# Performance work log

Hardware: AMD Instinct MI355X
Metric: run time of the kernel (lower is better)

## Reference

```python
import jax, jax.numpy as jnp
import numpy as np

N_QUBITS = 12
RANK = 1024
K = 4            # outcomes per qubit
D = 2 ** N_QUBITS
N_IDX = 1_000_000


def setup_inputs() -> dict:
    key = jax.random.key(0)
    k1, k2, k3, k4 = jax.random.split(key, 4)
    params = jax.random.normal(k1, (2, D, RANK), dtype=jnp.float32)
    M_real = jax.random.normal(k2, (K, 2, 2), dtype=jnp.float32)
    M_imag = jax.random.normal(k3, (K, 2, 2), dtype=jnp.float32)
    P_idxs = jax.random.randint(k4, (N_IDX,), 0, K ** N_QUBITS, dtype=jnp.int64)
    return {"params": params, "M_real": M_real, "M_imag": M_imag, "P_idxs": P_idxs}


def _qmt(rho, M, n_qubits):
    """Born rule: P[s1..sN] = Tr[(M_{s1} x ... x M_{sN}) rho].
    Sequential per-qubit contraction; T has shape [K^n, 2^(N-n), 2^(N-n)]."""
    T = rho[None, :, :]  # axes: (done outcomes, row legs j, col legs i)
    for _ in range(n_qubits):
        k, r, c = T.shape[0], T.shape[1] // 2, T.shape[2] // 2
        Tt = T.reshape(k, 2, r, 2, c)  # (k, j_n, j_rest, i_n, i_rest)
        # Tr contribution: sum_{i,j} M[s,i,j] * rho[j,i]
        T = jnp.einsum('sij,kjait->ksat', M, Tt).reshape(k * M.shape[0], r, c)
    return T.reshape(-1)  # [K^N] complex


def reference(params, M_real, M_imag, P_idxs):
    # rho = U U^H / Tr(U U^H)
    U = jax.lax.complex(params[0], params[1])            # [D, RANK] complex64
    rho = U @ U.conj().T                                  # [D, D]
    rho = rho / jnp.trace(rho)
    M = jax.lax.complex(M_real, M_imag)                   # [K, 2, 2] complex64
    P_all = _qmt(rho, M, N_QUBITS).real                   # [K^N] float32
    return P_all[P_idxs]
```

## Files before the change

### kernel.cpp

```cpp
#include <hip/hip_runtime.h>

#define D 4096
#define RANK 1024
#define K2 2048
#define UELEMS 4194304ULL
#define NTOT 16777216ULL
#define QSCALE 16000.0f

typedef __attribute__((ext_vector_type(4))) int i32x4;

__device__ float g_inv_tr[1];
__device__ float g_scale[D];

static __device__ __forceinline__ void load_lds16(const void* g, void* l) {
    __builtin_amdgcn_global_load_lds(
        (const __attribute__((address_space(1))) unsigned int*)g,
        (__attribute__((address_space(3))) unsigned int*)l, 16, 0, 0);
}

__global__ __launch_bounds__(256) void convert_w_i8(const float* __restrict__ P,
                                                    char* __restrict__ Wh,
                                                    char* __restrict__ Wl,
                                                    char* __restrict__ N2h,
                                                    char* __restrict__ N2l)
{
    const int w = threadIdx.x >> 6, lane = threadIdx.x & 63;
    const int row = blockIdx.x * 4 + w;

    float ur[16], ui[16];
    const float* pr = P + (size_t)row * RANK + lane * 16;
    const float* pi = P + UELEMS + (size_t)row * RANK + lane * 16;
    #pragma unroll
    for (int q = 0; q < 4; ++q) {
        const float4 a = ((const float4*)pr)[q];
        const float4 b = ((const float4*)pi)[q];
        ur[q * 4 + 0] = a.x; ur[q * 4 + 1] = a.y; ur[q * 4 + 2] = a.z; ur[q * 4 + 3] = a.w;
        ui[q * 4 + 0] = b.x; ui[q * 4 + 1] = b.y; ui[q * 4 + 2] = b.z; ui[q * 4 + 3] = b.w;
    }
    float mx = 0.f;
    #pragma unroll
    for (int e = 0; e < 16; ++e)
        mx = fmaxf(mx, fmaxf(fabsf(ur[e]), fabsf(ui[e])));
    #pragma unroll
    for (int off = 1; off < 64; off <<= 1)
        mx = fmaxf(mx, __shfl_xor(mx, off));
    const float inv = mx > 0.f ? QSCALE / mx : 0.f;
    if (lane == 0) g_scale[row] = mx / QSCALE;

    int hr[16], lr[16], hi[16], li[16];
    #pragma unroll
    for (int e = 0; e < 16; ++e) {
        float q = ur[e] * inv;
        float hf = rintf(q * 0.0078125f);
        hr[e] = (int)hf; lr[e] = (int)rintf(q - 128.f * hf);
        q = ui[e] * inv;
        hf = rintf(q * 0.0078125f);
        hi[e] = (int)hf; li[e] = (int)rintf(q - 128.f * hf);
    }
    uint4 phr, plr, phi, pli, pnh, pnl;
    unsigned* dst[6] = {(unsigned*)&phr, (unsigned*)&plr, (unsigned*)&phi,
                        (unsigned*)&pli, (unsigned*)&pnh, (unsigned*)&pnl};
    #pragma unroll
    for (int q = 0; q < 4; ++q) {
        unsigned a = 0, b = 0, c = 0, d = 0, e = 0, f = 0;
        #pragma unroll
        for (int k = 0; k < 4; ++k) {
            const int sh = k * 8;
            a |= (unsigned)(hr[q * 4 + k] & 255) << sh;
            b |= (unsigned)(lr[q * 4 + k] & 255) << sh;
            c |= (unsigned)(hi[q * 4 + k] & 255) << sh;
            d |= (unsigned)(li[q * 4 + k] & 255) << sh;
            e |= (unsigned)((-hi[q * 4 + k]) & 255) << sh;
            f |= (unsigned)((-li[q * 4 + k]) & 255) << sh;
        }
        dst[0][q] = a; dst[1][q] = b; dst[2][q] = c; dst[3][q] = d; dst[4][q] = e; dst[5][q] = f;
    }
    const size_t b1 = (size_t)row * 2048 + lane * 16;
    *(uint4*)&Wh[b1] = phr;          *(uint4*)&Wl[b1] = plr;
    *(uint4*)&Wh[b1 + 1024] = phi;   *(uint4*)&Wl[b1 + 1024] = pli;
    const size_t b2 = (size_t)row * 1024 + lane * 16;
    *(uint4*)&N2h[b2] = pnh;         *(uint4*)&N2l[b2] = pnl;
}

__global__ __launch_bounds__(256, 2) void gemm_rho_i8(const char* __restrict__ Wh,
                                                      const char* __restrict__ Wl,
                                                      const char* __restrict__ N2h,
                                                      const char* __restrict__ N2l,
                                                      float2* __restrict__ rho)
{
    __shared__ __align__(16) char sA1h[64 * 64];
    __shared__ __align__(16) char sA1l[64 * 64];
    __shared__ __align__(16) char sA2h[64 * 64];
    __shared__ __align__(16) char sA2l[64 * 64];
    __shared__ __align__(16) char sB1h[128 * 64];
    __shared__ __align__(16) char sB1l[128 * 64];
    __shared__ __align__(16) char sB2h[128 * 64];
    __shared__ __align__(16) char sB2l[128 * 64];
    __shared__ __align__(16) char sN2h[128 * 64];
    __shared__ __align__(16) char sN2l[128 * 64];

    const int b = blockIdx.x;
    int bj = (int)((65.0f - sqrtf(4225.0f - 4.0f * (float)b)) * 0.5f);
    while (bj > 0 && bj * (65 - bj) > b) --bj;
    while ((bj + 1) * (64 - bj) <= b) ++bj;
    const int bi = 2 * bj + (b - bj * (65 - bj));
    const int row0 = bi << 6, col0 = bj << 7;
    const bool full = (bi >= 2 * bj + 2);

    const int t = threadIdx.x;
    const int lane = t & 63, w = t >> 6;
    const int wr = w >> 1, wc = w & 1;

    const int rowA = t >> 2;
    const int kcA = (t & 3) ^ ((rowA >> 1) & 3);
    const size_t aoff = (size_t)(row0 + rowA) * 2048 + kcA * 16;
    const int ldsA = t * 16;
    size_t boff[2], boffN[2]; int ldsB[2];
    #pragma unroll
    for (int q = 0; q < 2; ++q) {
        const int g = q * 256 + t;
        const int rowB = g >> 2;
        const int kcB = (g & 3) ^ ((rowB >> 1) & 3);
        boff[q]  = (size_t)(col0 + rowB) * 2048 + kcB * 16;
        boffN[q] = (size_t)(col0 + rowB) * 1024 + kcB * 16;
        ldsB[q] = g * 16;
    }

    const int m = lane & 15, gq = lane >> 4;
    const int fko = (gq ^ ((m >> 1) & 3)) * 16;

    i32x4 rehh[2][4], remx[2][4], imhh[2][4], immx[2][4];
    #pragma unroll
    for (int i = 0; i < 2; ++i)
        #pragma unroll
        for (int j = 0; j < 4; ++j) {
            rehh[i][j] = (i32x4){0, 0, 0, 0}; remx[i][j] = (i32x4){0, 0, 0, 0};
            imhh[i][j] = (i32x4){0, 0, 0, 0}; immx[i][j] = (i32x4){0, 0, 0, 0};
        }

    for (int kt = 0; kt < RANK; kt += 64) {
        load_lds16(Wh + aoff + kt,        &sA1h[ldsA]);
        load_lds16(Wl + aoff + kt,        &sA1l[ldsA]);
        load_lds16(Wh + aoff + kt + 1024, &sA2h[ldsA]);
        load_lds16(Wl + aoff + kt + 1024, &sA2l[ldsA]);
        #pragma unroll
        for (int q = 0; q < 2; ++q) {
            load_lds16(Wh + boff[q] + kt,        &sB1h[ldsB[q]]);
            load_lds16(Wl + boff[q] + kt,        &sB1l[ldsB[q]]);
            load_lds16(Wh + boff[q] + kt + 1024, &sB2h[ldsB[q]]);
            load_lds16(Wl + boff[q] + kt + 1024, &sB2l[ldsB[q]]);
            load_lds16(N2h + boffN[q] + kt,      &sN2h[ldsB[q]]);
            load_lds16(N2l + boffN[q] + kt,      &sN2l[ldsB[q]]);
        }
        __syncthreads();

        i32x4 fa1h[2], fa1l[2], fa2h[2], fa2l[2];
        #pragma unroll
        for (int i = 0; i < 2; ++i) {
            const int off = (wr * 32 + i * 16 + m) * 64 + fko;
            fa1h[i] = *(const i32x4*)&sA1h[off];
            fa1l[i] = *(const i32x4*)&sA1l[off];
            fa2h[i] = *(const i32x4*)&sA2h[off];
            fa2l[i] = *(const i32x4*)&sA2l[off];
        }
        #pragma unroll
        for (int j = 0; j < 4; ++j) {
            const int off = (wc * 64 + j * 16 + m) * 64 + fko;
            const i32x4 b1h = *(const i32x4*)&sB1h[off];
            const i32x4 b1l = *(const i32x4*)&sB1l[off];
            const i32x4 b2h = *(const i32x4*)&sB2h[off];
            const i32x4 b2l = *(const i32x4*)&sB2l[off];
            const i32x4 n2h = *(const i32x4*)&sN2h[off];
            const i32x4 n2l = *(const i32x4*)&sN2l[off];
            #pragma unroll
            for (int i = 0; i < 2; ++i) {
                i32x4 r = rehh[i][j];
                r = __builtin_amdgcn_mfma_i32_16x16x64_i8(fa1h[i], b1h, r, 0, 0, 0);
                r = __builtin_amdgcn_mfma_i32_16x16x64_i8(fa2h[i], b2h, r, 0, 0, 0);
                rehh[i][j] = r;
                r = remx[i][j];
                r = __builtin_amdgcn_mfma_i32_16x16x64_i8(fa1h[i], b1l, r, 0, 0, 0);
                r = __builtin_amdgcn_mfma_i32_16x16x64_i8(fa1l[i], b1h, r, 0, 0, 0);
                r = __builtin_amdgcn_mfma_i32_16x16x64_i8(fa2h[i], b2l, r, 0, 0, 0);
                r = __builtin_amdgcn_mfma_i32_16x16x64_i8(fa2l[i], b2h, r, 0, 0, 0);
                remx[i][j] = r;
                r = imhh[i][j];
                r = __builtin_amdgcn_mfma_i32_16x16x64_i8(fa2h[i], b1h, r, 0, 0, 0);
                r = __builtin_amdgcn_mfma_i32_16x16x64_i8(fa1h[i], n2h, r, 0, 0, 0);
                imhh[i][j] = r;
                r = immx[i][j];
                r = __builtin_amdgcn_mfma_i32_16x16x64_i8(fa2h[i], b1l, r, 0, 0, 0);
                r = __builtin_amdgcn_mfma_i32_16x16x64_i8(fa2l[i], b1h, r, 0, 0, 0);
                r = __builtin_amdgcn_mfma_i32_16x16x64_i8(fa1h[i], n2l, r, 0, 0, 0);
                r = __builtin_amdgcn_mfma_i32_16x16x64_i8(fa1l[i], n2h, r, 0, 0, 0);
                immx[i][j] = r;
            }
        }
        __syncthreads();
    }

    #pragma unroll
    for (int i = 0; i < 2; ++i)
        #pragma unroll
        for (int j = 0; j < 4; ++j) {
            const int col = col0 + wc * 64 + j * 16 + m;
            const float sc = g_scale[col];
            #pragma unroll
            for (int r = 0; r < 4; ++r) {
                const int row = row0 + wr * 32 + i * 16 + gq * 4 + r;
                const float s2 = g_scale[row] * sc;
                const float re = s2 * (16384.f * (float)rehh[i][j][r] + 128.f * (float)remx[i][j][r]);
                const float im = s2 * (16384.f * (float)imhh[i][j][r] + 128.f * (float)immx[i][j][r]);
                if (full || row >= col) rho[(size_t)row * D + col] = make_float2(re, im);
                if (full || row > col)  rho[(size_t)col * D + row] = make_float2(re, -im);
            }
        }
}

__global__ void trace_inv(const float2* __restrict__ rho)
{
    __shared__ float red[256];
    float s = 0.f;
    for (int d = threadIdx.x; d < D; d += 256)
        s += rho[(size_t)d * (D + 1)].x;
    red[threadIdx.x] = s;
    __syncthreads();
    for (int off = 128; off > 0; off >>= 1) {
        if (threadIdx.x < off) red[threadIdx.x] += red[threadIdx.x + off];
        __syncthreads();
    }
    if (threadIdx.x == 0) g_inv_tr[0] = 1.0f / red[0];
}

static __device__ __forceinline__ void qmt2(float2* x,
                                            const float* __restrict__ Mre,
                                            const float* __restrict__ Mim)
{
    float2 y[16];
    #pragma unroll
    for (int sb = 0; sb < 4; ++sb)
        #pragma unroll
        for (int ja = 0; ja < 2; ++ja)
            #pragma unroll
            for (int ia = 0; ia < 2; ++ia) {
                float2 acc = make_float2(0.f, 0.f);
                #pragma unroll
                for (int ib = 0; ib < 2; ++ib)
                    #pragma unroll
                    for (int jb = 0; jb < 2; ++jb) {
                        const float mr = Mre[sb * 4 + ib * 2 + jb];
                        const float mi = Mim[sb * 4 + ib * 2 + jb];
                        const float2 v = x[(ja * 2 + jb) * 4 + ia * 2 + ib];
                        acc.x += mr * v.x - mi * v.y;
                        acc.y += mr * v.y + mi * v.x;
                    }
                y[sb * 4 + ja * 2 + ia] = acc;
            }
    #pragma unroll
    for (int sa = 0; sa < 4; ++sa)
        #pragma unroll
        for (int sb = 0; sb < 4; ++sb) {
            float2 acc = make_float2(0.f, 0.f);
            #pragma unroll
            for (int ia = 0; ia < 2; ++ia)
                #pragma unroll
                for (int ja = 0; ja < 2; ++ja) {
                    const float mr = Mre[sa * 4 + ia * 2 + ja];
                    const float mi = Mim[sa * 4 + ia * 2 + ja];
                    const float2 v = y[sb * 4 + ja * 2 + ia];
                    acc.x += mr * v.x - mi * v.y;
                    acc.y += mr * v.y + mi * v.x;
                }
            x[sa * 4 + sb] = acc;
        }
}

__global__ __launch_bounds__(256) void qmt_pA(const float2* __restrict__ in,
                                              float2* __restrict__ out,
                                              const float* __restrict__ Mre,
                                              const float* __restrict__ Mim)
{
    __shared__ __align__(16) float2 X[256 * 17];
    const int t = threadIdx.x;
    const int grp = blockIdx.x;
    const int rr = grp >> 6, cc = grp & 63;

    const int a4 = t >> 4, t4 = t & 15;
    float2 x[16];
    #pragma unroll
    for (int j2 = 0; j2 < 4; ++j2) {
        const float2* p = in + ((size_t)(rr * 64 + a4 * 4 + j2)) * 4096 + cc * 64 + t4 * 4;
        const float4 v0 = ((const float4*)p)[0];
        const float4 v1 = ((const float4*)p)[1];
        x[j2 * 4 + 0] = make_float2(v0.x, v0.y);
        x[j2 * 4 + 1] = make_float2(v0.z, v0.w);
        x[j2 * 4 + 2] = make_float2(v1.x, v1.y);
        x[j2 * 4 + 3] = make_float2(v1.z, v1.w);
    }
    qmt2(x, Mre, Mim);
    #pragma unroll
    for (int d = 0; d < 16; ++d) X[t * 17 + d] = x[d];
    __syncthreads();

    const int a2 = t >> 6, t2 = (t >> 4) & 3, d1 = t & 15;
    #pragma unroll
    for (int j2 = 0; j2 < 4; ++j2)
        #pragma unroll
        for (int i2 = 0; i2 < 4; ++i2)
            x[j2 * 4 + i2] = X[((a2 * 4 + j2) * 16 + t2 * 4 + i2) * 17 + d1];
    __syncthreads();
    qmt2(x, Mre, Mim);
    #pragma unroll
    for (int d = 0; d < 16; ++d) X[(a2 * 4 + t2) * 257 + d * 16 + d1] = x[d];
    __syncthreads();

    const int e2 = t >> 4, e1 = t & 15;
    #pragma unroll
    for (int j2 = 0; j2 < 4; ++j2)
        #pragma unroll
        for (int i2 = 0; i2 < 4; ++i2)
            x[j2 * 4 + i2] = X[(j2 * 4 + i2) * 257 + e2 * 16 + e1];
    qmt2(x, Mre, Mim);
    const size_t ob = (size_t)grp * 4096 + e2 * 16 + e1;
    #pragma unroll
    for (int d = 0; d < 16; ++d) out[ob + (size_t)d * 256] = x[d];
}

static __device__ __forceinline__ void qmt_stage_cb(float2* x,
                                                    const float* __restrict__ Mre,
                                                    const float* __restrict__ Mim)
{
    #pragma unroll
    for (int jj = 0; jj < 4; ++jj) {
        float2 y[16];
        #pragma unroll
        for (int sc = 0; sc < 4; ++sc)
            #pragma unroll
            for (int ii = 0; ii < 4; ++ii) {
                float2 acc = make_float2(0.f, 0.f);
                #pragma unroll
                for (int ic = 0; ic < 2; ++ic)
                    #pragma unroll
                    for (int jc = 0; jc < 2; ++jc) {
                        const float mr = Mre[sc * 4 + ic * 2 + jc];
                        const float mi = Mim[sc * 4 + ic * 2 + jc];
                        const float2 v = x[jj * 16 + jc * 8 + ii * 2 + ic];
                        acc.x += mr * v.x - mi * v.y;
                        acc.y += mr * v.y + mi * v.x;
                    }
                y[sc * 4 + ii] = acc;
            }
        #pragma unroll
        for (int q = 0; q < 16; ++q) x[jj * 16 + q] = y[q];
    }

    #pragma unroll
    for (int ja = 0; ja < 2; ++ja)
        #pragma unroll
        for (int sc = 0; sc < 4; ++sc) {
            float2 z[8];
            #pragma unroll
            for (int sb = 0; sb < 4; ++sb)
                #pragma unroll
                for (int ia = 0; ia < 2; ++ia) {
                    float2 acc = make_float2(0.f, 0.f);
                    #pragma unroll
                    for (int ib = 0; ib < 2; ++ib)
                        #pragma unroll
                        for (int jb = 0; jb < 2; ++jb) {
                            const float mr = Mre[sb * 4 + ib * 2 + jb];
                            const float mi = Mim[sb * 4 + ib * 2 + jb];
                            const float2 v = x[(ja * 2 + jb) * 16 + sc * 4 + ia * 2 + ib];
                            acc.x += mr * v.x - mi * v.y;
                            acc.y += mr * v.y + mi * v.x;
                        }
                    z[sb * 2 + ia] = acc;
                }
            #pragma unroll
            for (int sb = 0; sb < 4; ++sb)
                #pragma unroll
                for (int ia = 0; ia < 2; ++ia)
                    x[ja * 32 + (sb >> 1) * 16 + sc * 4 + ia * 2 + (sb & 1)] = z[sb * 2 + ia];
        }
}

#define QMT_STAGE_A(STORE)                                                     \
    _Pragma("unroll")                                                          \
    for (int sbH = 0; sbH < 2; ++sbH)                                          \
        _Pragma("unroll")                                                      \
        for (int sc = 0; sc < 4; ++sc)                                         \
            _Pragma("unroll")                                                  \
            for (int sbL = 0; sbL < 2; ++sbL) {                                \
                const int sb = sbH * 2 + sbL;                                  \
                _Pragma("unroll")                                              \
                for (int sa = 0; sa < 4; ++sa) {                               \
                    float2 acc = make_float2(0.f, 0.f);                        \
                    _Pragma("unroll")                                          \
                    for (int ia = 0; ia < 2; ++ia)                             \
                        _Pragma("unroll")                                      \
                        for (int ja = 0; ja < 2; ++ja) {                       \
                            const float mr = Mre[sa * 4 + ia * 2 + ja];        \
                            const float mi = Mim[sa * 4 + ia * 2 + ja];        \
                            const float2 v = x[ja * 32 + sbH * 16 + sc * 4 + ia * 2 + sbL]; \
                            acc.x += mr * v.x - mi * v.y;                      \
                            acc.y += mr * v.y + mi * v.x;                      \
                        }                                                      \
                    const int s3 = sa * 16 + sb * 4 + sc;                      \
                    STORE;                                                     \
                }                                                              \
            }

__global__ __launch_bounds__(256) void qmt_p3(const float2* __restrict__ in,
                                              float2* __restrict__ out,
                                              const float* __restrict__ Mre,
                                              const float* __restrict__ Mim)
{
    const int tid = blockIdx.x * 256 + threadIdx.x;
    const int s = tid & 4095, c3 = (tid >> 12) & 7, r3 = tid >> 15;

    float2 x[64];
    #pragma unroll
    for (int j3 = 0; j3 < 8; ++j3)
        #pragma unroll
        for (int i3 = 0; i3 < 8; ++i3)
            x[j3 * 8 + i3] = in[(size_t)((r3 * 8 + j3) * 64 + c3 * 8 + i3) * 4096 + s];
    qmt_stage_cb(x, Mre, Mim);
    const size_t ob = ((size_t)(r3 * 8 + c3) * 64) * 4096 + s;
    QMT_STAGE_A(out[ob + s3 * 4096] = acc)
}

__global__ __launch_bounds__(256) void qmt_p4(const float2* __restrict__ in,
                                              float* __restrict__ out,
                                              const float* __restrict__ Mre,
                                              const float* __restrict__ Mim)
{
    const int tid = blockIdx.x * 256 + threadIdx.x;
    float2 x[64];
    #pragma unroll
    for (int j3 = 0; j3 < 8; ++j3)
        #pragma unroll
        for (int i3 = 0; i3 < 8; ++i3)
            x[j3 * 8 + i3] = in[(size_t)(j3 * 8 + i3) * 262144 + tid];
    qmt_stage_cb(x, Mre, Mim);
    const size_t ob = (size_t)(tid >> 5) * 2048 + (tid & 31);
    QMT_STAGE_A(out[ob + s3 * 32] = acc.x)
}

__global__ void gather_idx(const float* __restrict__ P, const int* __restrict__ idxs,
                           float* __restrict__ out, const int n)
{
    const int i = blockIdx.x * 256 + threadIdx.x;
    if (i < n) {
        const int idx = idxs[i];
        const int s = idx & 262143;
        const size_t pos = (size_t)(s >> 5) * 2048 + (size_t)(idx >> 18) * 32 + (s & 31);
        out[i] = P[pos] * g_inv_tr[0];
    }
}

extern "C" void kernel_launch(void* const* d_in, const int* in_sizes, int n_in,
                              void* d_out, int out_size, void* d_ws, size_t ws_size,
                              hipStream_t stream)
{
    const float* params = (const float*)d_in[0];
    const float* Mre    = (const float*)d_in[1];
    const float* Mim    = (const float*)d_in[2];
    const int*   idxs   = (const int*)d_in[3];
    float*       out    = (float*)d_out;

    float* ws = (float*)d_ws;
    float2* A  = (float2*)ws;
    float2* Bp = (float2*)(ws + 2 * NTOT);
    char* Wh  = (char*)Bp;
    char* Wl  = Wh + (size_t)D * 2048;
    char* N2h = Wl + (size_t)D * 2048;
    char* N2l = N2h + (size_t)D * 1024;

    convert_w_i8<<<1024, 256, 0, stream>>>(params, Wh, Wl, N2h, N2l);
    gemm_rho_i8<<<1056, 256, 0, stream>>>(Wh, Wl, N2h, N2l, A);
    trace_inv<<<1, 256, 0, stream>>>(A);

    qmt_pA<<<4096, 256, 0, stream>>>(A, Bp, Mre, Mim);
    qmt_p3<<<1024, 256, 0, stream>>>(Bp, A, Mre, Mim);
    qmt_p4<<<1024, 256, 0, stream>>>(A, (float*)Bp, Mre, Mim);

    gather_idx<<<(out_size + 255) / 256, 256, 0, stream>>>((float*)Bp, idxs, out, out_size);
}
```

Before: 449.6 us.

## Exploit Hermitian symmetry of rho to halve first QMT pass reads

After: 433.7 us. -3.5%, faster.

```diff
diff --git a/kernel.cpp b/kernel.cpp
--- a/kernel.cpp
+++ b/kernel.cpp
@@ -11,6 +11,8 @@
 
 __device__ float g_inv_tr[1];
 __device__ float g_scale[D];
+__device__ float g_mdre[16];
+__device__ float g_mdim[16];
 
 static __device__ __forceinline__ void load_lds16(const void* g, void* l) {
     __builtin_amdgcn_global_load_lds(
@@ -19,11 +21,19 @@
 }
 
 __global__ __launch_bounds__(256) void convert_w_i8(const float* __restrict__ P,
+                                                    const float* __restrict__ Mre,
+                                                    const float* __restrict__ Mim,
                                                     char* __restrict__ Wh,
                                                     char* __restrict__ Wl,
                                                     char* __restrict__ N2h,
                                                     char* __restrict__ N2l)
 {
+    if (blockIdx.x == 0 && threadIdx.x < 16) {
+        const int s = threadIdx.x >> 2, i = (threadIdx.x >> 1) & 1, j = threadIdx.x & 1;
+        g_mdre[threadIdx.x] =  Mre[s * 4 + j * 2 + i];
+        g_mdim[threadIdx.x] = -Mim[s * 4 + j * 2 + i];
+    }
+
     const int w = threadIdx.x >> 6, lane = threadIdx.x & 63;
     const int row = blockIdx.x * 4 + w;
 
@@ -212,7 +222,8 @@
                 const float re = s2 * (16384.f * (float)rehh[i][j][r] + 128.f * (float)remx[i][j][r]);
                 const float im = s2 * (16384.f * (float)imhh[i][j][r] + 128.f * (float)immx[i][j][r]);
                 if (full || row >= col) rho[(size_t)row * D + col] = make_float2(re, im);
-                if (full || row > col)  rho[(size_t)col * D + row] = make_float2(re, -im);
+                if (row > col && ((row >> 6) == (col >> 6)))
+                    rho[(size_t)col * D + row] = make_float2(re, -im);
             }
         }
 }
@@ -275,55 +286,78 @@
         }
 }
 
-__global__ __launch_bounds__(256) void qmt_pA(const float2* __restrict__ in,
-                                              float2* __restrict__ out,
-                                              const float* __restrict__ Mre,
-                                              const float* __restrict__ Mim)
+static __device__ __forceinline__ void pA_pipeline(float2* x, float2* X, const int t,
+                                                   const float* __restrict__ mre,
+                                                   const float* __restrict__ mim)
+{
+    qmt2(x, mre, mim);
+    #pragma unroll
+    for (int d = 0; d < 16; ++d) X[t * 17 + d] = x[d];
+    __syncthreads();
+    const int a2 = t >> 6, t2 = (t >> 4) & 3, d1 = t & 15;
+    #pragma unroll
+    for (int j2 = 0; j2 < 4; ++j2)
+        #pragma unroll
+        for (int i2 = 0; i2 < 4; ++i2)
+            x[j2 * 4 + i2] = X[((a2 * 4 + j2) * 16 + t2 * 4 + i2) * 17 + d1];
+    __syncthreads();
+    qmt2(x, mre, mim);
+    #pragma unroll
+    for (int d = 0; d < 16; ++d) X[(a2 * 4 + t2) * 257 + d * 16 + d1] = x[d];
+    __syncthreads();
+    const int e2 = t >> 4, e1 = t & 15;
+    #pragma unroll
+    for (int j2 = 0; j2 < 4; ++j2)
+        #pragma unroll
+        for (int i2 = 0; i2 < 4; ++i2)
+            x[j2 * 4 + i2] = X[(j2 * 4 + i2) * 257 + e2 * 16 + e1];
+    qmt2(x, mre, mim);
+}
+
+__global__ __launch_bounds__(256) void qmt_pAh(const float2* __restrict__ in,
+                                               float2* __restrict__ out,
+                                               const float* __restrict__ Mre,
+                                               const float* __restrict__ Mim)
 {
     __shared__ __align__(16) float2 X[256 * 17];
     const int t = threadIdx.x;
-    const int grp = blockIdx.x;
-    const int rr = grp >> 6, cc = grp & 63;
+    const int g = blockIdx.x;
+    int rr = (int)((sqrtf(8.f * (float)g + 1.f) - 1.f) * 0.5f);
+    while (rr * (rr + 1) / 2 > g) --rr;
+    while ((rr + 1) * (rr + 2) / 2 <= g) ++rr;
+    const int cc = g - rr * (rr + 1) / 2;
 
     const int a4 = t >> 4, t4 = t & 15;
-    float2 x[16];
+    float2 x0[16], x[16];
     #pragma unroll
     for (int j2 = 0; j2 < 4; ++j2) {
         const float2* p = in + ((size_t)(rr * 64 + a4 * 4 + j2)) * 4096 + cc * 64 + t4 * 4;
         const float4 v0 = ((const float4*)p)[0];
         const float4 v1 = ((const float4*)p)[1];
-        x[j2 * 4 + 0] = make_float2(v0.x, v0.y);
-        x[j2 * 4 + 1] = make_float2(v0.z, v0.w);
-        x[j2 * 4 + 2] = make_float2(v1.x, v1.y);
-        x[j2 * 4 + 3] = make_float2(v1.z, v1.w);
-    }
-    qmt2(x, Mre, Mim);
-    #pragma unroll
-    for (int d = 0; d < 16; ++d) X[t * 17 + d] = x[d];
-    __syncthreads();
-
-    const int a2 = t >> 6, t2 = (t >> 4) & 3, d1 = t & 15;
-    #pragma unroll
-    for (int j2 = 0; j2 < 4; ++j2)
-        #pragma unroll
-        for (int i2 = 0; i2 < 4; ++i2)
-            x[j2 * 4 + i2] = X[((a2 * 4 + j2) * 16 + t2 * 4 + i2) * 17 + d1];
-    __syncthreads();
-    qmt2(x, Mre, Mim);
-    #pragma unroll
-    for (int d = 0; d < 16; ++d) X[(a2 * 4 + t2) * 257 + d * 16 + d1] = x[d];
-    __syncthreads();
-
+        x0[j2 * 4 + 0] = make_float2(v0.x, v0.y);
+        x0[j2 * 4 + 1] = make_float2(v0.z, v0.w);
+        x0[j2 * 4 + 2] = make_float2(v1.x, v1.y);
+        x0[j2 * 4 + 3] = make_float2(v1.z, v1.w);
+    }
+
+    #pragma unroll
+    for (int q = 0; q < 16; ++q) x[q] = x0[q];
+    pA_pipeline(x, X, t, Mre, Mim);
     const int e2 = t >> 4, e1 = t & 15;
-    #pragma unroll
-    for (int j2 = 0; j2 < 4; ++j2)
-        #pragma unroll
-        for (int i2 = 0; i2 < 4; ++i2)
-            x[j2 * 4 + i2] = X[(j2 * 4 + i2) * 257 + e2 * 16 + e1];
-    qmt2(x, Mre, Mim);
-    const size_t ob = (size_t)grp * 4096 + e2 * 16 + e1;
-    #pragma unroll
-    for (int d = 0; d < 16; ++d) out[ob + (size_t)d * 256] = x[d];
+    const size_t ob0 = (size_t)(rr * 64 + cc) * 4096 + e2 * 16 + e1;
+    #pragma unroll
+    for (int d = 0; d < 16; ++d) out[ob0 + (size_t)d * 256] = x[d];
+
+    if (rr != cc) {
+        __syncthreads();
+        #pragma unroll
+        for (int q = 0; q < 16; ++q) x[q] = x0[q];
+        pA_pipeline(x, X, t, g_mdre, g_mdim);
+        const size_t ob1 = (size_t)(cc * 64 + rr) * 4096 + e2 * 16 + e1;
+        #pragma unroll
+        for (int d = 0; d < 16; ++d)
+            out[ob1 + (size_t)d * 256] = make_float2(x[d].x, -x[d].y);
+    }
 }
 
 static __device__ __forceinline__ void qmt_stage_cb(float2* x,
@@ -476,11 +510,11 @@
     char* N2h = Wl + (size_t)D * 2048;
     char* N2l = N2h + (size_t)D * 1024;
 
-    convert_w_i8<<<1024, 256, 0, stream>>>(params, Wh, Wl, N2h, N2l);
+    convert_w_i8<<<1024, 256, 0, stream>>>(params, Mre, Mim, Wh, Wl, N2h, N2l);
     gemm_rho_i8<<<1056, 256, 0, stream>>>(Wh, Wl, N2h, N2l, A);
     trace_inv<<<1, 256, 0, stream>>>(A);
 
-    qmt_pA<<<4096, 256, 0, stream>>>(A, Bp, Mre, Mim);
+    qmt_pAh<<<2080, 256, 0, stream>>>(A, Bp, Mre, Mim);
     qmt_p3<<<1024, 256, 0, stream>>>(Bp, A, Mre, Mim);
     qmt_p4<<<1024, 256, 0, stream>>>(A, (float*)Bp, Mre, Mim);
 
```
